# Performance work log

Measured on AMD Instinct MI355X. Metric: run time of the kernel, lower is better.

The kernel has to match this reference:

```python
import jax, jax.numpy as jnp
import numpy as np

N_LAYERS = 3
EMB_DIM = 64
N_MASHUP = 100000
N_API = 50000
N_EDGES_MASHUP = 3200000
N_EDGES_API = 1600000
EPS = 1e-12  # F.normalize clamp_min epsilon


def setup_inputs() -> dict:
    key = jax.random.key(0)
    ks = jax.random.split(key, 8)
    return {
        "adj_mashup_rows": jax.random.randint(ks[0], (N_EDGES_MASHUP,), 0, N_MASHUP, dtype=jnp.int32),
        "adj_mashup_cols": jax.random.randint(ks[1], (N_EDGES_MASHUP,), 0, N_MASHUP, dtype=jnp.int32),
        "adj_mashup_vals": jax.random.uniform(ks[2], (N_EDGES_MASHUP,), dtype=jnp.float32),
        "adj_api_rows": jax.random.randint(ks[3], (N_EDGES_API,), 0, N_API, dtype=jnp.int32),
        "adj_api_cols": jax.random.randint(ks[4], (N_EDGES_API,), 0, N_API, dtype=jnp.int32),
        "adj_api_vals": jax.random.uniform(ks[5], (N_EDGES_API,), dtype=jnp.float32),
        "mashup_emb": jax.random.normal(ks[6], (N_MASHUP, EMB_DIM), dtype=jnp.float32),
        "api_emb": jax.random.normal(ks[7], (N_API, EMB_DIM), dtype=jnp.float32),
    }


def _spmm(rows, cols, vals, x, n_nodes):
    # sparse [n,n] @ dense [n,d] via gather + weighted segment-sum
    return jax.ops.segment_sum(vals[:, None] * x[cols], rows, num_segments=n_nodes)


def _propagate(rows, cols, vals, emb):
    n = emb.shape[0]
    acc = emb
    cur = emb
    for _ in range(N_LAYERS):
        cur = _spmm(rows, cols, vals, cur, n)
        acc = acc + cur
    out = acc / (N_LAYERS + 1)  # mean over stacked layers (incl. layer 0)
    norm = jnp.maximum(jnp.linalg.norm(out, axis=1, keepdims=True), EPS)
    return out / norm


def reference(adj_mashup_rows, adj_mashup_cols, adj_mashup_vals,
              adj_api_rows, adj_api_cols, adj_api_vals,
              mashup_emb, api_emb):
    final_mashup = _propagate(adj_mashup_rows, adj_mashup_cols, adj_mashup_vals, mashup_emb)
    final_api = _propagate(adj_api_rows, adj_api_cols, adj_api_vals, api_emb)
    return final_mashup, final_api
```

## Files before the change

### kernel.cpp

```cpp
#include <hip/hip_runtime.h>


#define EMB_DIM 64
#define UNR 8
typedef unsigned long long ull;
typedef int v4i __attribute__((ext_vector_type(4)));

static inline int cdiv(long long a, long long b) { return (int)((a + b - 1) / b); }


__global__ void k_zero2(int* __restrict__ pm, int nm_, int* __restrict__ pa,
                        int na_) {
    int i = blockIdx.x * blockDim.x + threadIdx.x;
    if (i < nm_) pm[i] = 0;
    else if (i < nm_ + na_) pa[i - nm_] = 0;
}

__global__ void k_hist2(const int* __restrict__ rm, int nem,
                        int* __restrict__ posm, const int* __restrict__ ra,
                        int nea, int* __restrict__ posa) {
    int nm4 = nem >> 2, na4 = nea >> 2;
    int i = blockIdx.x * blockDim.x + threadIdx.x;
    if (i < nm4) {
        v4i r = __builtin_nontemporal_load((const v4i*)rm + i);
        atomicAdd(&posm[r.x], 1);
        atomicAdd(&posm[r.y], 1);
        atomicAdd(&posm[r.z], 1);
        atomicAdd(&posm[r.w], 1);
    } else if (i < nm4 + na4) {
        v4i r = __builtin_nontemporal_load((const v4i*)ra + (i - nm4));
        atomicAdd(&posa[r.x], 1);
        atomicAdd(&posa[r.y], 1);
        atomicAdd(&posa[r.z], 1);
        atomicAdd(&posa[r.w], 1);
    } else if (i == nm4 + na4) {
        for (int t = nm4 << 2; t < nem; ++t) atomicAdd(&posm[rm[t]], 1);
        for (int t = na4 << 2; t < nea; ++t) atomicAdd(&posa[ra[t]], 1);
    }
}

#define SCAN_B 256
#define SCAN_E 1024

__global__ void k_scan1m(const int* __restrict__ inm, int nm_,
                         int* __restrict__ outm, int* __restrict__ bsm,
                         int nsbm, const int* __restrict__ ina, int na_,
                         int* __restrict__ outa, int* __restrict__ bsa) {
    bool is_m = (int)blockIdx.x < nsbm;
    const int* in = is_m ? inm : ina;
    int* out = is_m ? outm : outa;
    int* bsums = is_m ? bsm : bsa;
    int n = is_m ? nm_ : na_;
    int b = is_m ? blockIdx.x : blockIdx.x - nsbm;

    __shared__ int lds[SCAN_B];
    int t = threadIdx.x;
    int base = b * SCAN_E + t * 4;
    int v[4];
    int s = 0;
#pragma unroll
    for (int j = 0; j < 4; ++j) {
        v[j] = (base + j < n) ? in[base + j] : 0;
        s += v[j];
    }
    lds[t] = s;
    __syncthreads();
    for (int off = 1; off < SCAN_B; off <<= 1) {
        int x = (t >= off) ? lds[t - off] : 0;
        __syncthreads();
        lds[t] += x;
        __syncthreads();
    }
    int run = lds[t] - s;
    if (t == SCAN_B - 1) bsums[b] = lds[t];
#pragma unroll
    for (int j = 0; j < 4; ++j) {
        if (base + j < n) out[base + j] = run;
        run += v[j];
    }
}

__global__ void k_scan2m(int* __restrict__ bsm, int nbm, int* __restrict__ bsa,
                         int nba) {
    int* bsums = (blockIdx.x == 0) ? bsm : bsa;
    int nb = (blockIdx.x == 0) ? nbm : nba;
    __shared__ int lds[1024];
    int t = threadIdx.x;
    int v = (t < nb) ? bsums[t] : 0;
    lds[t] = v;
    __syncthreads();
    for (int off = 1; off < 1024; off <<= 1) {
        int x = (t >= off) ? lds[t - off] : 0;
        __syncthreads();
        lds[t] += x;
        __syncthreads();
    }
    if (t < nb) bsums[t] = lds[t] - v;
}

__global__ void k_scan3m(int* __restrict__ rpm, int* __restrict__ posm,
                         const int* __restrict__ bsm, int nm_, int nem,
                         int* __restrict__ rpa, int* __restrict__ posa,
                         const int* __restrict__ bsa, int na_, int nea) {
    int i = blockIdx.x * blockDim.x + threadIdx.x;
    if (i < nm_) {
        int p = rpm[i] + bsm[i >> 10];
        rpm[i] = p;
        posm[i] = p;
        if (i == 0) rpm[nm_] = nem;
    } else if (i < nm_ + na_) {
        int ii = i - nm_;
        int p = rpa[ii] + bsa[ii >> 10];
        rpa[ii] = p;
        posa[ii] = p;
        if (ii == 0) rpa[na_] = nea;
    }
}

__global__ void k_scatter2(const int* __restrict__ rm,
                           const int* __restrict__ cm,
                           const float* __restrict__ vm, int nem,
                           unsigned pmulm, int* __restrict__ posm,
                           ull* __restrict__ evm, const int* __restrict__ ra,
                           const int* __restrict__ ca,
                           const float* __restrict__ va, int nea,
                           unsigned pmula, int* __restrict__ posa,
                           ull* __restrict__ eva, int bm) {
    const int p = blockIdx.x & 7;
    const bool is_m = (int)blockIdx.x < bm;
    const int b = is_m ? blockIdx.x : blockIdx.x - bm;
    const int nslot = (is_m ? bm : (int)gridDim.x - bm) >> 3;
    const int bslot = b >> 3;

    const int* rows = is_m ? rm : ra;
    const int* cols = is_m ? cm : ca;
    const float* vals = is_m ? vm : va;
    const int ne = is_m ? nem : nea;
    const unsigned pmul = is_m ? pmulm : pmula;
    int* row_pos = is_m ? posm : posa;
    ull* ev = is_m ? evm : eva;

    const int nb4 = ne >> 2;
    const v4i* rows4 = (const v4i*)rows;

    for (int g = bslot * blockDim.x + threadIdx.x; g < nb4;
         g += nslot * blockDim.x) {
        v4i r4 = __builtin_nontemporal_load(rows4 + g);
        int base = g << 2;
#pragma unroll
        for (int k = 0; k < 4; ++k) {
            int r = (k == 0) ? r4.x : (k == 1) ? r4.y : (k == 2) ? r4.z : r4.w;
            if ((int)(((unsigned)r * pmul) >> 16) == p) {
                int i = base + k;
                float v = __builtin_nontemporal_load(vals + i);
                int c = __builtin_nontemporal_load(cols + i);
                ull pk = ((ull)__float_as_uint(v) << 32) | (unsigned)c;
                int pos = atomicAdd(&row_pos[r], 1);
                ev[pos] = pk;
            }
        }
    }
    if (bslot == 0 && threadIdx.x == 0) {
        for (int i = nb4 << 2; i < ne; ++i) {
            int r = rows[i];
            if ((int)(((unsigned)r * pmul) >> 16) == p) {
                ull pk = ((ull)__float_as_uint(vals[i]) << 32) |
                         (unsigned)cols[i];
                int pos = atomicAdd(&row_pos[r], 1);
                ev[pos] = pk;
            }
        }
    }
}


__global__ void k_tohalf2(const float* __restrict__ sm, _Float16* __restrict__ dm,
                          int nm4, const float* __restrict__ sa,
                          _Float16* __restrict__ da, int na4) {
    int i = blockIdx.x * blockDim.x + threadIdx.x;
    const float* s;
    _Float16* d;
    int j;
    if (i < nm4) {
        s = sm; d = dm; j = i;
    } else if (i < nm4 + na4) {
        s = sa; d = da; j = i - nm4;
    } else {
        return;
    }
    float4 v = *reinterpret_cast<const float4*>(s + j * 4);
    _Float16 h[4] = {(_Float16)v.x, (_Float16)v.y, (_Float16)v.z,
                     (_Float16)v.w};
    *reinterpret_cast<ushort4*>(d + j * 4) = *reinterpret_cast<ushort4*>(h);
}

template <bool FIRST, bool LAST>
__device__ __forceinline__ void spmm_row(const ull* __restrict__ ev,
                                         const int* __restrict__ row_ptr,
                                         const _Float16* __restrict__ x,
                                         _Float16* __restrict__ nxt,
                                         float* __restrict__ acc,
                                         const float* __restrict__ emb,
                                         int row, int lane) {
    int q = lane >> 4;
    int sub = lane & 15;

    int s = row_ptr[row];
    int cnt = row_ptr[row + 1] - s;
    const ull* evr = ev + s;

    float a0[UNR], a1[UNR], a2[UNR], a3[UNR];
#pragma unroll
    for (int k = 0; k < UNR; ++k) {
        a0[k] = 0.f; a1[k] = 0.f; a2[k] = 0.f; a3[k] = 0.f;
    }

    int j = 0;
    for (; j + 4 * UNR <= cnt; j += 4 * UNR) {
        ull p[UNR];
#pragma unroll
        for (int k = 0; k < UNR; ++k)
            p[k] = __builtin_nontemporal_load(evr + j + 4 * k + q);
#pragma unroll
        for (int k = 0; k < UNR; ++k) {
            unsigned c = (unsigned)p[k];
            ull xd = *reinterpret_cast<const ull*>(
                x + ((size_t)c << 6) + (sub << 2));
            float v = __uint_as_float((unsigned)(p[k] >> 32));
            union { ull u; _Float16 f[4]; } cv;
            cv.u = xd;
            a0[k] = fmaf(v, (float)cv.f[0], a0[k]);
            a1[k] = fmaf(v, (float)cv.f[1], a1[k]);
            a2[k] = fmaf(v, (float)cv.f[2], a2[k]);
            a3[k] = fmaf(v, (float)cv.f[3], a3[k]);
        }
    }
    if (j < cnt) {
        ull p[UNR];
        bool act[UNR];
#pragma unroll
        for (int k = 0; k < UNR; ++k) {
            int slot = j + 4 * k + q;
            act[k] = slot < cnt;
            p[k] = act[k] ? __builtin_nontemporal_load(evr + slot) : 0ull;
        }
#pragma unroll
        for (int k = 0; k < UNR; ++k) {
            if (act[k]) {
                unsigned c = (unsigned)p[k];
                ull xd = *reinterpret_cast<const ull*>(
                    x + ((size_t)c << 6) + (sub << 2));
                float v = __uint_as_float((unsigned)(p[k] >> 32));
                union { ull u; _Float16 f[4]; } cv;
                cv.u = xd;
                a0[k] = fmaf(v, (float)cv.f[0], a0[k]);
                a1[k] = fmaf(v, (float)cv.f[1], a1[k]);
                a2[k] = fmaf(v, (float)cv.f[2], a2[k]);
                a3[k] = fmaf(v, (float)cv.f[3], a3[k]);
            }
        }
    }
    float t0 = 0.f, t1 = 0.f, t2 = 0.f, t3 = 0.f;
#pragma unroll
    for (int k = 0; k < UNR; ++k) {
        t0 += a0[k]; t1 += a1[k]; t2 += a2[k]; t3 += a3[k];
    }
    t0 += __shfl_xor(t0, 16); t0 += __shfl_xor(t0, 32);
    t1 += __shfl_xor(t1, 16); t1 += __shfl_xor(t1, 32);
    t2 += __shfl_xor(t2, 16); t2 += __shfl_xor(t2, 32);
    t3 += __shfl_xor(t3, 16); t3 += __shfl_xor(t3, 32);

    size_t base = ((size_t)row << 6) + (sub << 2);
    if (FIRST || !LAST) {
        if (q == 0) {
            float4 prev;
            if (FIRST)
                prev = *reinterpret_cast<const float4*>(emb + base);
            else
                prev = *reinterpret_cast<const float4*>(acc + base);
            float4 o = make_float4(prev.x + t0, prev.y + t1, prev.z + t2,
                                   prev.w + t3);
            *reinterpret_cast<float4*>(acc + base) = o;
            union { _Float16 f[4]; ull u; } h;
            h.f[0] = (_Float16)t0; h.f[1] = (_Float16)t1;
            h.f[2] = (_Float16)t2; h.f[3] = (_Float16)t3;
            *reinterpret_cast<ull*>(nxt + base) = h.u;
        }
    } else {
        float4 a2v = *reinterpret_cast<const float4*>(acc + base);
        float b0 = (a2v.x + t0) * 0.25f;
        float b1 = (a2v.y + t1) * 0.25f;
        float b2 = (a2v.z + t2) * 0.25f;
        float b3 = (a2v.w + t3) * 0.25f;
        float ss = b0 * b0 + b1 * b1 + b2 * b2 + b3 * b3;
#pragma unroll
        for (int off = 8; off; off >>= 1) ss += __shfl_xor(ss, off);
        float nrm = fmaxf(sqrtf(ss), 1e-12f);
        if (q == 0) {
            float4 o = make_float4(b0 / nrm, b1 / nrm, b2 / nrm, b3 / nrm);
            *reinterpret_cast<float4*>(acc + base) = o;
        }
    }
}

template <bool FIRST, bool LAST>
__global__ void k_spmm2(const ull* __restrict__ evm,
                        const int* __restrict__ rpm,
                        const _Float16* __restrict__ xm,
                        _Float16* __restrict__ nxm, float* __restrict__ accm,
                        const float* __restrict__ embm, int nm_,
                        const ull* __restrict__ eva,
                        const int* __restrict__ rpa,
                        const _Float16* __restrict__ xa,
                        _Float16* __restrict__ nxa, float* __restrict__ acca,
                        const float* __restrict__ emba, int na_) {
    int wid = (int)((blockIdx.x * blockDim.x + threadIdx.x) >> 6);
    int lane = threadIdx.x & 63;
    if (wid < nm_) {
        spmm_row<FIRST, LAST>(evm, rpm, xm, nxm, accm, embm, wid, lane);
    } else if (wid < nm_ + na_) {
        spmm_row<FIRST, LAST>(eva, rpa, xa, nxa, acca, emba, wid - nm_, lane);
    }
}


__global__ void k_copy2(const float4* __restrict__ src, float4* __restrict__ a,
                        float4* __restrict__ b, int n4) {
    int i = blockIdx.x * blockDim.x + threadIdx.x;
    if (i < n4) {
        float4 v = src[i];
        a[i] = v;
        b[i] = v;
    }
}

__global__ void k_zero(float4* __restrict__ p, int n4) {
    int i = blockIdx.x * blockDim.x + threadIdx.x;
    if (i < n4) p[i] = make_float4(0.f, 0.f, 0.f, 0.f);
}

__global__ void k_axpy(float4* __restrict__ acc, const float4* __restrict__ x,
                       int n4) {
    int i = blockIdx.x * blockDim.x + threadIdx.x;
    if (i < n4) {
        float4 a = acc[i];
        float4 v = x[i];
        a.x += v.x; a.y += v.y; a.z += v.z; a.w += v.w;
        acc[i] = a;
    }
}

__global__ void k_spmm_atomic(const int* __restrict__ rows,
                              const int* __restrict__ cols,
                              const float* __restrict__ vals,
                              const float* __restrict__ x,
                              float* __restrict__ y, int n_edges) {
    unsigned tid = blockIdx.x * blockDim.x + threadIdx.x;
    unsigned e = tid >> 4;
    if (e >= (unsigned)n_edges) return;
    int sub = tid & 15;
    int r = rows[e];
    int c = cols[e];
    float v = vals[e];
    const float4 xv =
        *reinterpret_cast<const float4*>(x + ((size_t)c << 6) + (sub << 2));
    float* yp = y + ((size_t)r << 6) + (sub << 2);
    unsafeAtomicAdd(yp + 0, v * xv.x);
    unsafeAtomicAdd(yp + 1, v * xv.y);
    unsafeAtomicAdd(yp + 2, v * xv.z);
    unsafeAtomicAdd(yp + 3, v * xv.w);
}

__global__ void k_normalize(float* __restrict__ out, int nrows) {
    int row = blockIdx.x * 4 + (threadIdx.x >> 6);
    if (row >= nrows) return;
    int lane = threadIdx.x & 63;
    size_t idx = ((size_t)row << 6) + lane;
    float v = out[idx] * 0.25f;
    float s = v * v;
#pragma unroll
    for (int off = 32; off; off >>= 1) s += __shfl_xor(s, off);
    float norm = fmaxf(sqrtf(s), 1e-12f);
    out[idx] = v / norm;
}


extern "C" void kernel_launch(void* const* d_in, const int* in_sizes, int n_in,
                              void* d_out, int out_size, void* d_ws,
                              size_t ws_size, hipStream_t stream) {
    const int* m_rows = (const int*)d_in[0];
    const int* m_cols = (const int*)d_in[1];
    const float* m_vals = (const float*)d_in[2];
    const int* a_rows = (const int*)d_in[3];
    const int* a_cols = (const int*)d_in[4];
    const float* a_vals = (const float*)d_in[5];
    const float* m_emb = (const float*)d_in[6];
    const float* a_emb = (const float*)d_in[7];

    int ne_m = in_sizes[0];
    int ne_a = in_sizes[3];
    int nm = in_sizes[6] / EMB_DIM;
    int na = in_sizes[7] / EMB_DIM;

    size_t elems_m = (size_t)nm * EMB_DIM;
    size_t elems_a = (size_t)na * EMB_DIM;
    float* out_m = (float*)d_out;
    float* out_a = out_m + elems_m;

    char* w = (char*)d_ws;
    ull* ev_m = (ull*)w;            w += (size_t)ne_m * sizeof(ull);
    ull* ev_a = (ull*)w;            w += (size_t)ne_a * sizeof(ull);
    _Float16* x0h_m = (_Float16*)w; w += elems_m * sizeof(_Float16);
    _Float16* buf_m = (_Float16*)w; w += elems_m * sizeof(_Float16);
    _Float16* x0h_a = (_Float16*)w; w += elems_a * sizeof(_Float16);
    _Float16* buf_a = (_Float16*)w; w += elems_a * sizeof(_Float16);
    int* row_ptr_m = (int*)w;       w += ((size_t)nm + 1) * sizeof(int);
    int* row_ptr_a = (int*)w;       w += ((size_t)na + 1) * sizeof(int);
    size_t need = (size_t)(w - (char*)d_ws);

    int* row_pos_m = (int*)x0h_m;
    int* row_pos_a = row_pos_m + nm;
    int* bsums_m = row_pos_a + na;
    int* bsums_a = bsums_m + 1024;
    bool alias_ok = ((size_t)nm + na + 2048) * sizeof(int) <=
                    elems_m * sizeof(_Float16);

    if (ws_size >= need && alias_ok) {
        k_zero2<<<cdiv(nm + na, 256), 256, 0, stream>>>(row_pos_m, nm,
                                                        row_pos_a, na);
        k_hist2<<<cdiv((ne_m >> 2) + (ne_a >> 2) + 1, 256), 256, 0, stream>>>(
            m_rows, ne_m, row_pos_m, a_rows, ne_a, row_pos_a);
        int nsb_m = cdiv(nm, SCAN_E);
        int nsb_a = cdiv(na, SCAN_E);
        k_scan1m<<<nsb_m + nsb_a, SCAN_B, 0, stream>>>(
            row_pos_m, nm, row_ptr_m, bsums_m, nsb_m, row_pos_a, na,
            row_ptr_a, bsums_a);
        k_scan2m<<<2, 1024, 0, stream>>>(bsums_m, nsb_m, bsums_a, nsb_a);
        k_scan3m<<<cdiv(nm + na, 256), 256, 0, stream>>>(
            row_ptr_m, row_pos_m, bsums_m, nm, ne_m, row_ptr_a, row_pos_a,
            bsums_a, na, ne_a);
        unsigned pmul_m = (unsigned)(((unsigned long long)8 << 16) / (unsigned)nm);
        unsigned pmul_a = (unsigned)(((unsigned long long)8 << 16) / (unsigned)na);
        k_scatter2<<<2048, 256, 0, stream>>>(m_rows, m_cols, m_vals, ne_m,
                                             pmul_m, row_pos_m, ev_m, a_rows,
                                             a_cols, a_vals, ne_a, pmul_a,
                                             row_pos_a, ev_a, 1408);
        int nm4 = (int)(elems_m / 4), na4 = (int)(elems_a / 4);
        k_tohalf2<<<cdiv(nm4 + na4, 256), 256, 0, stream>>>(
            m_emb, x0h_m, nm4, a_emb, x0h_a, na4);
        int g = cdiv(nm + na, 4);
        k_spmm2<true, false><<<g, 256, 0, stream>>>(
            ev_m, row_ptr_m, x0h_m, buf_m, out_m, m_emb, nm,
            ev_a, row_ptr_a, x0h_a, buf_a, out_a, a_emb, na);
        k_spmm2<false, false><<<g, 256, 0, stream>>>(
            ev_m, row_ptr_m, buf_m, x0h_m, out_m, nullptr, nm,
            ev_a, row_ptr_a, buf_a, x0h_a, out_a, nullptr, na);
        k_spmm2<false, true><<<g, 256, 0, stream>>>(
            ev_m, row_ptr_m, x0h_m, nullptr, out_m, nullptr, nm,
            ev_a, row_ptr_a, x0h_a, nullptr, out_a, nullptr, na);
        return;
    }

    float* fb0 = (float*)d_ws;
    float* fb1 = fb0 + elems_m;
    auto run_atomic = [&](const int* rows, const int* cols, const float* vals,
                          const float* emb, float* out, int nrows,
                          int nedges) {
        size_t n = (size_t)nrows * EMB_DIM;
        int n4 = (int)(n / 4);
        int eg = cdiv(n4, 256);
        k_copy2<<<eg, 256, 0, stream>>>((const float4*)emb, (float4*)out,
                                        (float4*)fb0, n4);
        float* cur = fb0;
        float* nxt = fb1;
        int spmm_grid = cdiv((long long)nedges * 16, 256);
        for (int l = 0; l < 3; ++l) {
            k_zero<<<eg, 256, 0, stream>>>((float4*)nxt, n4);
            k_spmm_atomic<<<spmm_grid, 256, 0, stream>>>(rows, cols, vals, cur,
                                                         nxt, nedges);
            k_axpy<<<eg, 256, 0, stream>>>((float4*)out, (const float4*)nxt,
                                           n4);
            float* t = cur; cur = nxt; nxt = t;
        }
        k_normalize<<<cdiv(nrows, 4), 256, 0, stream>>>(out, nrows);
    };
    run_atomic(m_rows, m_cols, m_vals, m_emb, out_m, nm, ne_m);
    run_atomic(a_rows, a_cols, a_vals, a_emb, out_a, na, ne_a);
}
```

Baseline: 950.8 us.

## Replace direct COO scatter with two-pass bucketed scatter via LDS staging

The single-pass scatter, which did per-edge global atomics into random row positions, is replaced by a two-pass radix-style bucketing. Pass one groups edges into 512-row buckets, staging them in LDS and flushing 8-element aligned chunks to a temporary buffer with one atomic per bucket per tile. Pass two scatters each bucket locally, so the atomics and writes land in a small, cache-resident region. This trades an extra read and write of the edge list, plus more kernels and workspace aliasing, for better locality in the scatter.

```diff
diff --git a/kernel.cpp b/kernel.cpp
--- a/kernel.cpp
+++ b/kernel.cpp
@@ -3,8 +3,11 @@
 
 #define EMB_DIM 64
 #define UNR 8
+#define RPB_SH 9
+#define NBMAX 256
 typedef unsigned long long ull;
 typedef int v4i __attribute__((ext_vector_type(4)));
+typedef float v4f __attribute__((ext_vector_type(4)));
 
 static inline int cdiv(long long a, long long b) { return (int)((a + b - 1) / b); }
 
@@ -117,58 +120,161 @@
     }
 }
 
-__global__ void k_scatter2(const int* __restrict__ rm,
-                           const int* __restrict__ cm,
-                           const float* __restrict__ vm, int nem,
-                           unsigned pmulm, int* __restrict__ posm,
-                           ull* __restrict__ evm, const int* __restrict__ ra,
-                           const int* __restrict__ ca,
-                           const float* __restrict__ va, int nea,
-                           unsigned pmula, int* __restrict__ posa,
-                           ull* __restrict__ eva, int bm) {
-    const int p = blockIdx.x & 7;
+__global__ void k_binit2(const int* __restrict__ rpm, int NBm,
+                         int* __restrict__ curm, int* __restrict__ tbm,
+                         const int* __restrict__ rpa, int NBa,
+                         int* __restrict__ cura, int* __restrict__ tba) {
+    int t = blockIdx.x * blockDim.x + threadIdx.x;
+    if (t < NBm) {
+        int base = (rpm[t << RPB_SH] & ~7) + 8 * t;
+        curm[t] = base;
+        tbm[t] = base;
+    } else if (t < NBm + NBa) {
+        int b = t - NBm;
+        int base = (rpa[b << RPB_SH] & ~7) + 8 * b;
+        cura[b] = base;
+        tba[b] = base;
+    }
+}
+
+__global__ __launch_bounds__(512) void k_pass1(
+    const int* __restrict__ rm, const int* __restrict__ cm,
+    const float* __restrict__ vm, int nem, int* __restrict__ curm,
+    ull* __restrict__ tmpm, int NBm, const int* __restrict__ ra,
+    const int* __restrict__ ca, const float* __restrict__ va, int nea,
+    int* __restrict__ cura, ull* __restrict__ tmpa, int NBa, int bm) {
+    __shared__ int l_cnt[NBMAX], l_tile[NBMAX], l_base[NBMAX], l_nf[NBMAX];
+    __shared__ ull l_buf[NBMAX][8];
+
     const bool is_m = (int)blockIdx.x < bm;
-    const int b = is_m ? blockIdx.x : blockIdx.x - bm;
-    const int nslot = (is_m ? bm : (int)gridDim.x - bm) >> 3;
-    const int bslot = b >> 3;
-
     const int* rows = is_m ? rm : ra;
     const int* cols = is_m ? cm : ca;
     const float* vals = is_m ? vm : va;
     const int ne = is_m ? nem : nea;
-    const unsigned pmul = is_m ? pmulm : pmula;
-    int* row_pos = is_m ? posm : posa;
-    ull* ev = is_m ? evm : eva;
-
-    const int nb4 = ne >> 2;
-    const v4i* rows4 = (const v4i*)rows;
-
-    for (int g = bslot * blockDim.x + threadIdx.x; g < nb4;
-         g += nslot * blockDim.x) {
-        v4i r4 = __builtin_nontemporal_load(rows4 + g);
-        int base = g << 2;
-#pragma unroll
-        for (int k = 0; k < 4; ++k) {
-            int r = (k == 0) ? r4.x : (k == 1) ? r4.y : (k == 2) ? r4.z : r4.w;
-            if ((int)(((unsigned)r * pmul) >> 16) == p) {
-                int i = base + k;
-                float v = __builtin_nontemporal_load(vals + i);
-                int c = __builtin_nontemporal_load(cols + i);
-                ull pk = ((ull)__float_as_uint(v) << 32) | (unsigned)c;
-                int pos = atomicAdd(&row_pos[r], 1);
-                ev[pos] = pk;
+    const int NB = is_m ? NBm : NBa;
+    int* cursor = is_m ? curm : cura;
+    ull* tmp = is_m ? tmpm : tmpa;
+    const int nbk = is_m ? bm : (int)gridDim.x - bm;
+    const int blk = is_m ? blockIdx.x : blockIdx.x - bm;
+
+    int per = ((ne + nbk - 1) / nbk + 3) & ~3;
+    int c0 = blk * per;
+    int c1 = c0 + per;
+    if (c1 > ne) c1 = ne;
+    const int tid = threadIdx.x;
+
+    for (int b = tid; b < NB; b += 512) l_cnt[b] = 0;
+
+    for (int t0 = c0; t0 < c1; t0 += 2048) {
+        for (int b = tid; b < NB; b += 512) l_tile[b] = 0;
+        __syncthreads();
+
+        int i0 = t0 + tid * 4;
+        int bk[4];
+        ull it[4];
+        int ofs[4];
+        bool act[4];
+        if (i0 + 4 <= c1) {
+            v4i r4 = __builtin_nontemporal_load((const v4i*)(rows + i0));
+            v4i c4 = __builtin_nontemporal_load((const v4i*)(cols + i0));
+            v4f v4 = __builtin_nontemporal_load((const v4f*)(vals + i0));
+            int rr[4] = {r4.x, r4.y, r4.z, r4.w};
+            int cc[4] = {c4.x, c4.y, c4.z, c4.w};
+            float vv[4] = {v4.x, v4.y, v4.z, v4.w};
+#pragma unroll
+            for (int j = 0; j < 4; ++j) {
+                act[j] = true;
+                bk[j] = rr[j] >> RPB_SH;
+                unsigned lo = (unsigned)cc[j] |
+                              ((unsigned)(rr[j] & 511) << 17);
+                it[j] = ((ull)__float_as_uint(vv[j]) << 32) | lo;
             }
-        }
-    }
-    if (bslot == 0 && threadIdx.x == 0) {
-        for (int i = nb4 << 2; i < ne; ++i) {
-            int r = rows[i];
-            if ((int)(((unsigned)r * pmul) >> 16) == p) {
-                ull pk = ((ull)__float_as_uint(vals[i]) << 32) |
-                         (unsigned)cols[i];
-                int pos = atomicAdd(&row_pos[r], 1);
-                ev[pos] = pk;
+        } else {
+#pragma unroll
+            for (int j = 0; j < 4; ++j) {
+                int i = i0 + j;
+                act[j] = i < c1;
+                if (act[j]) {
+                    int r = rows[i];
+                    bk[j] = r >> RPB_SH;
+                    unsigned lo = (unsigned)cols[i] |
+                                  ((unsigned)(r & 511) << 17);
+                    it[j] = ((ull)__float_as_uint(vals[i]) << 32) | lo;
+                } else {
+                    bk[j] = 0;
+                }
             }
+        }
+#pragma unroll
+        for (int j = 0; j < 4; ++j)
+            if (act[j]) ofs[j] = atomicAdd(&l_tile[bk[j]], 1);
+        __syncthreads();
+
+        for (int b = tid; b < NB; b += 512) {
+            int tot = l_cnt[b] + l_tile[b];
+            int nf = tot & ~7;
+            l_nf[b] = nf;
+            if (nf > 0) l_base[b] = atomicAdd(&cursor[b], nf);
+        }
+        __syncthreads();
+
+        for (int b = tid; b < NB; b += 512) {
+            int nf = l_nf[b];
+            if (nf > 0) {
+                int old = l_cnt[b];
+                int gb = l_base[b];
+                for (int s = 0; s < old; ++s) tmp[gb + s] = l_buf[b][s];
+            }
+        }
+        __syncthreads();
+
+#pragma unroll
+        for (int j = 0; j < 4; ++j) {
+            if (act[j]) {
+                int b = bk[j];
+                int rank = l_cnt[b] + ofs[j];
+                int nf = l_nf[b];
+                if (rank < nf)
+                    tmp[l_base[b] + rank] = it[j];
+                else
+                    l_buf[b][rank - nf] = it[j];
+            }
+        }
+        __syncthreads();
+
+        for (int b = tid; b < NB; b += 512)
+            l_cnt[b] += l_tile[b] - l_nf[b];
+        __syncthreads();
+    }
+
+    for (int b = tid; b < NB; b += 512) {
+        int cnt = l_cnt[b];
+        if (cnt > 0) {
+            int gb = atomicAdd(&cursor[b], cnt);
+            for (int s = 0; s < cnt; ++s) tmp[gb + s] = l_buf[b][s];
+        }
+    }
+}
+
+__global__ void k_pass2(const ull* __restrict__ tmp,
+                        const int* __restrict__ tb,
+                        const int* __restrict__ rp, int NB, int n,
+                        int* __restrict__ pos, ull* __restrict__ ev) {
+    int p = blockIdx.x & 7;
+    int bslot = blockIdx.x >> 3;
+    int nslot = gridDim.x >> 3;
+    for (int b = p; b < NB; b += 8) {
+        int r0 = b << RPB_SH;
+        int r1 = r0 + (1 << RPB_SH);
+        if (r1 > n) r1 = n;
+        int cnt = rp[r1] - rp[r0];
+        int base = tb[b];
+        for (int i = bslot * 256 + threadIdx.x; i < cnt; i += nslot * 256) {
+            ull it = __builtin_nontemporal_load(tmp + base + i);
+            unsigned lo = (unsigned)it;
+            int row = r0 + (int)(lo >> 17);
+            int ps = atomicAdd(&pos[row], 1);
+            ev[ps] = (it & 0xFFFFFFFF00000000ull) | (ull)(lo & 0x1FFFFu);
         }
     }
 }
@@ -193,6 +299,7 @@
                      (_Float16)v.w};
     *reinterpret_cast<ushort4*>(d + j * 4) = *reinterpret_cast<ushort4*>(h);
 }
+
 
 template <bool FIRST, bool LAST>
 __device__ __forceinline__ void spmm_row(const ull* __restrict__ ev,
@@ -407,23 +514,41 @@
     float* out_m = (float*)d_out;
     float* out_a = out_m + elems_m;
 
+    int NB_m = cdiv(nm, 1 << RPB_SH);
+    int NB_a = cdiv(na, 1 << RPB_SH);
+
     char* w = (char*)d_ws;
     ull* ev_m = (ull*)w;            w += (size_t)ne_m * sizeof(ull);
     ull* ev_a = (ull*)w;            w += (size_t)ne_a * sizeof(ull);
-    _Float16* x0h_m = (_Float16*)w; w += elems_m * sizeof(_Float16);
-    _Float16* buf_m = (_Float16*)w; w += elems_m * sizeof(_Float16);
-    _Float16* x0h_a = (_Float16*)w; w += elems_a * sizeof(_Float16);
-    _Float16* buf_a = (_Float16*)w; w += elems_a * sizeof(_Float16);
+    char* U = w;                    w += (elems_m + elems_a) * 2 * sizeof(_Float16);
     int* row_ptr_m = (int*)w;       w += ((size_t)nm + 1) * sizeof(int);
     int* row_ptr_a = (int*)w;       w += ((size_t)na + 1) * sizeof(int);
     size_t need = (size_t)(w - (char*)d_ws);
 
-    int* row_pos_m = (int*)x0h_m;
+    _Float16* x0h_m = (_Float16*)U;
+    _Float16* buf_m = x0h_m + elems_m;
+    _Float16* x0h_a = buf_m + elems_m;
+    _Float16* buf_a = x0h_a + elems_a;
+
+    ull* tmp_m = (ull*)U;
+    size_t tmpm_extent = ((size_t)ne_m + 8 * NBMAX) * sizeof(ull);
+    char* meta = U + ((tmpm_extent + 1023) & ~(size_t)1023);
+    int* row_pos_m = (int*)meta;
     int* row_pos_a = row_pos_m + nm;
     int* bsums_m = row_pos_a + na;
     int* bsums_a = bsums_m + 1024;
-    bool alias_ok = ((size_t)nm + na + 2048) * sizeof(int) <=
-                    elems_m * sizeof(_Float16);
+    int* cur_m = bsums_a + 1024;
+    int* cur_a = cur_m + NBMAX;
+    int* tb_m = cur_a + NBMAX;
+    int* tb_a = tb_m + NBMAX;
+    size_t meta_end = (size_t)((char*)(tb_a + NBMAX) - U);
+    ull* tmp_a = ev_m;
+    size_t tmpa_extent = ((size_t)ne_a + 8 * NBMAX) * sizeof(ull);
+
+    bool alias_ok =
+        meta_end <= (elems_m + elems_a) * 2 * sizeof(_Float16) &&
+        tmpa_extent <= (size_t)ne_m * sizeof(ull) &&
+        NB_m <= NBMAX && NB_a <= NBMAX;
 
     if (ws_size >= need && alias_ok) {
         k_zero2<<<cdiv(nm + na, 256), 256, 0, stream>>>(row_pos_m, nm,
@@ -439,12 +564,15 @@
         k_scan3m<<<cdiv(nm + na, 256), 256, 0, stream>>>(
             row_ptr_m, row_pos_m, bsums_m, nm, ne_m, row_ptr_a, row_pos_a,
             bsums_a, na, ne_a);
-        unsigned pmul_m = (unsigned)(((unsigned long long)8 << 16) / (unsigned)nm);
-        unsigned pmul_a = (unsigned)(((unsigned long long)8 << 16) / (unsigned)na);
-        k_scatter2<<<2048, 256, 0, stream>>>(m_rows, m_cols, m_vals, ne_m,
-                                             pmul_m, row_pos_m, ev_m, a_rows,
-                                             a_cols, a_vals, ne_a, pmul_a,
-                                             row_pos_a, ev_a, 1408);
+        k_binit2<<<cdiv(NB_m + NB_a, 256), 256, 0, stream>>>(
+            row_ptr_m, NB_m, cur_m, tb_m, row_ptr_a, NB_a, cur_a, tb_a);
+        k_pass1<<<384, 512, 0, stream>>>(m_rows, m_cols, m_vals, ne_m, cur_m,
+                                         tmp_m, NB_m, a_rows, a_cols, a_vals,
+                                         ne_a, cur_a, tmp_a, NB_a, 256);
+        k_pass2<<<1024, 256, 0, stream>>>(tmp_a, tb_a, row_ptr_a, NB_a, na,
+                                          row_pos_a, ev_a);
+        k_pass2<<<2048, 256, 0, stream>>>(tmp_m, tb_m, row_ptr_m, NB_m, nm,
+                                          row_pos_m, ev_m);
         int nm4 = (int)(elems_m / 4), na4 = (int)(elems_a / 4);
         k_tohalf2<<<cdiv(nm4 + na4, 256), 256, 0, stream>>>(
             m_emb, x0h_m, nm4, a_emb, x0h_a, na4);
```

After: 1.019 ms. 1.07x slower.

## Replace global atomic row histogram with LDS-privatized partitioned histograms plus reduction

Applied to the files above, without the earlier changes.

The row-degree histogram no longer uses global atomics. Row ids are split into 16K-row partitions, and each block builds a packed 16-bit-pair histogram in LDS for one partition over a slice of the edges. The results go to slabs that alias the edge-value buffer, and a reduction kernel sums the slabs into row_pos. This removes contended global atomics and the zero kernel. In exchange, every block re-reads its edge slice once per partition (about 7 passes for mashup and 4 for api), and the 16-bit packed counts could overflow on a high-degree row.

```diff
diff --git a/kernel.cpp b/kernel.cpp
--- a/kernel.cpp
+++ b/kernel.cpp
@@ -3,41 +3,94 @@
 
 #define EMB_DIM 64
 #define UNR 8
+#define PSH 14
+#define HS_M 48
+#define HS_A 24
 typedef unsigned long long ull;
 typedef int v4i __attribute__((ext_vector_type(4)));
 
 static inline int cdiv(long long a, long long b) { return (int)((a + b - 1) / b); }
 
 
-__global__ void k_zero2(int* __restrict__ pm, int nm_, int* __restrict__ pa,
-                        int na_) {
-    int i = blockIdx.x * blockDim.x + threadIdx.x;
-    if (i < nm_) pm[i] = 0;
-    else if (i < nm_ + na_) pa[i - nm_] = 0;
-}
-
-__global__ void k_hist2(const int* __restrict__ rm, int nem,
-                        int* __restrict__ posm, const int* __restrict__ ra,
-                        int nea, int* __restrict__ posa) {
-    int nm4 = nem >> 2, na4 = nea >> 2;
-    int i = blockIdx.x * blockDim.x + threadIdx.x;
-    if (i < nm4) {
-        v4i r = __builtin_nontemporal_load((const v4i*)rm + i);
-        atomicAdd(&posm[r.x], 1);
-        atomicAdd(&posm[r.y], 1);
-        atomicAdd(&posm[r.z], 1);
-        atomicAdd(&posm[r.w], 1);
-    } else if (i < nm4 + na4) {
-        v4i r = __builtin_nontemporal_load((const v4i*)ra + (i - nm4));
-        atomicAdd(&posa[r.x], 1);
-        atomicAdd(&posa[r.y], 1);
-        atomicAdd(&posa[r.z], 1);
-        atomicAdd(&posa[r.w], 1);
-    } else if (i == nm4 + na4) {
-        for (int t = nm4 << 2; t < nem; ++t) atomicAdd(&posm[rm[t]], 1);
-        for (int t = na4 << 2; t < nea; ++t) atomicAdd(&posa[ra[t]], 1);
-    }
-}
+__global__ __launch_bounds__(512) void k_histlds(
+    const int* __restrict__ rm, int nem, int NPm, int Sm,
+    unsigned* __restrict__ slabm, const int* __restrict__ ra, int nea,
+    int NPa, int Sa, unsigned* __restrict__ slaba, int bm) {
+    __shared__ unsigned h[8192];
+
+    const bool is_m = (int)blockIdx.x < bm;
+    const int* rows = is_m ? rm : ra;
+    const int ne = is_m ? nem : nea;
+    const int NP = is_m ? NPm : NPa;
+    const int S = is_m ? Sm : Sa;
+    unsigned* slab = is_m ? slabm : slaba;
+    const int b = is_m ? blockIdx.x : blockIdx.x - bm;
+    const int p = b % NP;
+    const int slot = b / NP;
+    const int tid = threadIdx.x;
+
+    for (int i = tid; i < 8192; i += 512) h[i] = 0;
+    __syncthreads();
+
+    int chunk = ((ne + S - 1) / S + 3) & ~3;
+    int c0 = slot * chunk;
+    int c1 = c0 + chunk;
+    if (c1 > ne) c1 = ne;
+
+    for (int i0 = c0 + tid * 4; i0 < c1; i0 += 512 * 4) {
+        if (i0 + 4 <= c1) {
+            v4i r4 = __builtin_nontemporal_load((const v4i*)(rows + i0));
+            int rr[4] = {r4.x, r4.y, r4.z, r4.w};
+#pragma unroll
+            for (int j = 0; j < 4; ++j) {
+                int r = rr[j];
+                if ((r >> PSH) == p)
+                    atomicAdd(&h[(r & 16383) >> 1],
+                              (r & 1) ? 65536u : 1u);
+            }
+        } else {
+            for (int i = i0; i < c1; ++i) {
+                int r = rows[i];
+                if ((r >> PSH) == p)
+                    atomicAdd(&h[(r & 16383) >> 1],
+                              (r & 1) ? 65536u : 1u);
+            }
+        }
+    }
+    __syncthreads();
+
+    unsigned* dst = slab + ((size_t)(slot * NP + p) << 13);
+    for (int i = tid; i < 8192; i += 512)
+        __builtin_nontemporal_store(h[i], dst + i);
+}
+
+__global__ void k_histred(const unsigned* __restrict__ slabm, int NPm, int Sm,
+                          int nm_, int* __restrict__ posm,
+                          const unsigned* __restrict__ slaba, int NPa, int Sa,
+                          int na_, int* __restrict__ posa) {
+    int e = blockIdx.x * blockDim.x + threadIdx.x;
+    int em = NPm << 13;
+    const unsigned* slab;
+    int NP, S, n, p, k;
+    int* pos;
+    if (e < em) {
+        slab = slabm; NP = NPm; S = Sm; n = nm_; pos = posm;
+        p = e >> 13; k = e & 8191;
+    } else {
+        e -= em;
+        int ea = NPa << 13;
+        if (e >= ea) return;
+        slab = slaba; NP = NPa; S = Sa; n = na_; pos = posa;
+        p = e >> 13; k = e & 8191;
+    }
+    unsigned s = 0;
+    for (int slot = 0; slot < S; ++slot)
+        s += slab[((size_t)(slot * NP + p) << 13) + k];
+    int r0 = (p << PSH) + (k << 1);
+    if (r0 < n) pos[r0] = (int)(s & 0xFFFFu);
+    if (r0 + 1 < n) pos[r0 + 1] = (int)(s >> 16);
+}
+
 
 #define SCAN_B 256
 #define SCAN_E 1024
@@ -193,6 +246,7 @@
                      (_Float16)v.w};
     *reinterpret_cast<ushort4*>(d + j * 4) = *reinterpret_cast<ushort4*>(h);
 }
+
 
 template <bool FIRST, bool LAST>
 __device__ __forceinline__ void spmm_row(const ull* __restrict__ ev,
@@ -407,6 +461,9 @@
     float* out_m = (float*)d_out;
     float* out_a = out_m + elems_m;
 
+    int NP_m = cdiv(nm, 1 << PSH);
+    int NP_a = cdiv(na, 1 << PSH);
+
     char* w = (char*)d_ws;
     ull* ev_m = (ull*)w;            w += (size_t)ne_m * sizeof(ull);
     ull* ev_a = (ull*)w;            w += (size_t)ne_a * sizeof(ull);
@@ -425,11 +482,24 @@
     bool alias_ok = ((size_t)nm + na + 2048) * sizeof(int) <=
                     elems_m * sizeof(_Float16);
 
+    unsigned* slab_m = (unsigned*)ev_m;
+    unsigned* slab_a = (unsigned*)ev_a;
+    size_t slabm_bytes = (size_t)HS_M * NP_m * 8192 * sizeof(unsigned);
+    size_t slaba_bytes = (size_t)HS_A * NP_a * 8192 * sizeof(unsigned);
+    alias_ok = alias_ok && slabm_bytes <= (size_t)ne_m * sizeof(ull) &&
+               slaba_bytes <= (size_t)ne_a * sizeof(ull) && NP_m <= 16 &&
+               NP_a <= 16;
+
     if (ws_size >= need && alias_ok) {
-        k_zero2<<<cdiv(nm + na, 256), 256, 0, stream>>>(row_pos_m, nm,
-                                                        row_pos_a, na);
-        k_hist2<<<cdiv((ne_m >> 2) + (ne_a >> 2) + 1, 256), 256, 0, stream>>>(
-            m_rows, ne_m, row_pos_m, a_rows, ne_a, row_pos_a);
+        int hb_m = HS_M * NP_m;
+        int hb_a = HS_A * NP_a;
+        k_histlds<<<hb_m + hb_a, 512, 0, stream>>>(m_rows, ne_m, NP_m, HS_M,
+                                                   slab_m, a_rows, ne_a, NP_a,
+                                                   HS_A, slab_a, hb_m);
+        int red_threads = (NP_m + NP_a) * 8192;
+        k_histred<<<cdiv(red_threads, 256), 256, 0, stream>>>(
+            slab_m, NP_m, HS_M, nm, row_pos_m, slab_a, NP_a, HS_A, na,
+            row_pos_a);
         int nsb_m = cdiv(nm, SCAN_E);
         int nsb_a = cdiv(na, SCAN_E);
         k_scan1m<<<nsb_m + nsb_a, SCAN_B, 0, stream>>>(
```

Result: faster. 797.3 us (-16.1%).
